# Kernel tuning notes

Measured on AMD Instinct MI355X. Metric: run time of the kernel, lower is better.

Reference implementation:

```python
import jax, jax.numpy as jnp
import numpy as np

EMBED_DIM = 128
N_HEADS = 8
TANH_CLIP = 10.0
NEG_INF = -1e9


def setup_inputs() -> dict:
    key = jax.random.key(0)
    k1, k2, k3, k4 = jax.random.split(key, 4)
    B, N, D = 512, 200, EMBED_DIM
    s = 1.0 / np.sqrt(D)
    return {
        "embeddings": jax.random.normal(k1, (B, N, D), dtype=jnp.float32),
        "W_node": jax.random.uniform(k2, (D, 3 * D), jnp.float32, -s, s),
        "W_fixed": jax.random.uniform(k3, (D, D), jnp.float32, -s, s),
        "W_step": jax.random.uniform(k4, (D, D), jnp.float32, -s, s),
    }


def _decode(embeddings, W_node, W_fixed, W_step):
    B, N, D = embeddings.shape
    H = N_HEADS
    dk = D // H

    # Precompute (once): glimpse K/V and logit K, plus fixed graph context.
    proj = embeddings @ W_node                      # [B,N,3D]
    gK, gV, lK = jnp.split(proj, 3, axis=-1)
    gK = gK.reshape(B, N, H, dk).transpose(0, 2, 1, 3)   # [B,H,N,dk]
    gV = gV.reshape(B, N, H, dk).transpose(0, 2, 1, 3)   # [B,H,N,dk]
    graph_emb = embeddings.mean(axis=1)             # [B,D]
    fixed_ctx = graph_emb @ W_fixed                 # [B,D]

    inv_sqrt_dk = 1.0 / jnp.sqrt(jnp.asarray(dk, embeddings.dtype))
    inv_sqrt_d = 1.0 / jnp.sqrt(jnp.asarray(D, embeddings.dtype))
    batch_idx = jnp.arange(B)

    def step(carry, _):
        visited, ctx_emb = carry                    # [B,N] bool, [B,D]
        q = fixed_ctx + ctx_emb @ W_step            # [B,D]
        qh = q.reshape(B, H, dk)                    # [B,H,dk]
        # glimpse multi-head attention (mask_inner=True)
        compat = jnp.einsum('bhd,bhnd->bhn', qh, gK) * inv_sqrt_dk
        compat = jnp.where(visited[:, None, :], NEG_INF, compat)
        attn = jax.nn.softmax(compat, axis=-1)
        glimpse = jnp.einsum('bhn,bhnd->bhd', attn, gV).reshape(B, D)
        # single-head logits with tanh clipping (mask_logits=True)
        logits = jnp.einsum('bd,bnd->bn', glimpse, lK) * inv_sqrt_d
        logits = TANH_CLIP * jnp.tanh(logits)
        logits = jnp.where(visited, NEG_INF, logits)
        log_p = jax.nn.log_softmax(logits, axis=-1)  # [B,N]
        sel = jnp.argmax(log_p, axis=-1)             # greedy [B]
        visited = visited.at[batch_idx, sel].set(True)
        ctx_emb = embeddings[batch_idx, sel]         # next step context
        return (visited, ctx_emb), (log_p, sel)

    init = (jnp.zeros((B, N), dtype=bool), graph_emb)
    _, (log_ps, sels) = jax.lax.scan(step, init, None, length=N)
    return log_ps.transpose(1, 0, 2), sels.transpose(1, 0)  # [B,T,N], [B,T]


def reference(embeddings, W_node, W_fixed, W_step):
    log_p, pi = _decode(embeddings, W_node, W_fixed, W_step)
    return log_p, pi
```

## Files before the change

### kernel.cpp

```cpp
#include <hip/hip_runtime.h>
#include <math.h>


#define Bsz 512
#define Nn  200
#define Dd  128
#define TANH_CLIP 10.0f
#define NEG_INF  -1e9f
#define LOG2E 1.4426950408889634f
#define LN2   0.6931471805599453f
#define QSCALE (0.25f * LOG2E)
#define LSCALE (0.08838834764831845f * 2.0f * LOG2E)

typedef float v2f __attribute__((ext_vector_type(2)));

__device__ __forceinline__ v2f pkfma(v2f a, v2f b, v2f c) {
    return __builtin_elementwise_fma(a, b, c);
}
__device__ __forceinline__ float fast_rcp(float x) { return __builtin_amdgcn_rcpf(x); }
__device__ __forceinline__ float rdlane(float v, int l) {
    union { float f; int i; } u; u.f = v;
    u.i = __builtin_amdgcn_readlane(u.i, l);
    return u.f;
}

template <int CTRL, int RMASK, bool BC>
__device__ __forceinline__ float dppf(float x, float oldv) {
    int r = __builtin_amdgcn_update_dpp(__builtin_bit_cast(int, oldv),
                                        __builtin_bit_cast(int, x),
                                        CTRL, RMASK, 0xf, BC);
    return __builtin_bit_cast(float, r);
}
template <int CTRL, int RMASK, bool BC>
__device__ __forceinline__ int dppi(int x, int oldv) {
    return __builtin_amdgcn_update_dpp(oldv, x, CTRL, RMASK, 0xf, BC);
}
__device__ __forceinline__ float wave_sum63(float x) {
    x += dppf<0x111, 0xf, true >(x, 0.f);
    x += dppf<0x112, 0xf, true >(x, 0.f);
    x += dppf<0x114, 0xf, true >(x, 0.f);
    x += dppf<0x118, 0xf, true >(x, 0.f);
    x += dppf<0x142, 0xa, false>(x, 0.f);
    x += dppf<0x143, 0xc, false>(x, 0.f);
    return x;
}
__device__ __forceinline__ float wave_max63(float x) {
    x = fmaxf(x, dppf<0x111, 0xf, false>(x, -INFINITY));
    x = fmaxf(x, dppf<0x112, 0xf, false>(x, -INFINITY));
    x = fmaxf(x, dppf<0x114, 0xf, false>(x, -INFINITY));
    x = fmaxf(x, dppf<0x118, 0xf, false>(x, -INFINITY));
    x = fmaxf(x, dppf<0x142, 0xa, false>(x, -INFINITY));
    x = fmaxf(x, dppf<0x143, 0xc, false>(x, -INFINITY));
    return x;
}

__device__ __forceinline__ float dot16pk(const float4* g4, const float4* q4) {
    const v2f* g = (const v2f*)g4;
    const v2f* q = (const v2f*)q4;
    v2f a0 = g[0] * q[0];
    v2f a1 = g[1] * q[1];
    a0 = pkfma(g[2], q[2], a0);
    a1 = pkfma(g[3], q[3], a1);
    a0 = pkfma(g[4], q[4], a0);
    a1 = pkfma(g[5], q[5], a1);
    a0 = pkfma(g[6], q[6], a0);
    a1 = pkfma(g[7], q[7], a1);
    const v2f a = a0 + a1;
    return a.x + a.y;
}

__global__ __launch_bounds__(256, 3) void proj_kernel(
    const float* __restrict__ emb, const float* __restrict__ Wn,
    float* __restrict__ gk, float* __restrict__ gv, float* __restrict__ lk)
{
    const int bid = blockIdx.x;
    const int cg  = bid % 3;
    const int rowBase = (bid / 3) * 64;
    const int t  = threadIdx.x;
    const int c4 = t & 31;
    const int r8 = t >> 5;

    __shared__ __align__(16) float wn_s[64][128];
    __shared__ __align__(16) float e_s[64][68];

    float acc[8][4];
#pragma unroll
    for (int j = 0; j < 8; ++j)
#pragma unroll
        for (int m = 0; m < 4; ++m) acc[j][m] = 0.f;

    for (int kh = 0; kh < 2; ++kh) {
#pragma unroll
        for (int i = 0; i < 8; ++i) {
            const int idx = t + 256 * i;
            const int kr = idx >> 5, cc = (idx & 31) * 4;
            *(float4*)&wn_s[kr][cc] =
                *(const float4*)&Wn[(size_t)(kh * 64 + kr) * 384 + 128 * cg + cc];
        }
#pragma unroll
        for (int i = 0; i < 4; ++i) {
            const int idx = t + 256 * i;
            const int rr = idx >> 4, kk4 = (idx & 15) * 4;
            *(float4*)&e_s[rr][kk4] =
                *(const float4*)&emb[(size_t)(rowBase + rr) * Dd + kh * 64 + kk4];
        }
        __syncthreads();

#pragma unroll
        for (int k4 = 0; k4 < 16; ++k4) {
            float4 er[8];
#pragma unroll
            for (int j = 0; j < 8; ++j)
                er[j] = *(const float4*)&e_s[8 * r8 + j][4 * k4];
#pragma unroll
            for (int m = 0; m < 4; ++m) {
                const float4 wv = *(const float4*)&wn_s[4 * k4 + m][4 * c4];
#pragma unroll
                for (int j = 0; j < 8; ++j) {
                    const float ev = (m == 0) ? er[j].x : (m == 1) ? er[j].y
                                   : (m == 2) ? er[j].z : er[j].w;
                    acc[j][0] = fmaf(ev, wv.x, acc[j][0]);
                    acc[j][1] = fmaf(ev, wv.y, acc[j][1]);
                    acc[j][2] = fmaf(ev, wv.z, acc[j][2]);
                    acc[j][3] = fmaf(ev, wv.w, acc[j][3]);
                }
            }
        }
        __syncthreads();
    }

    float* out = (cg == 0) ? gk : (cg == 1) ? gv : lk;
    const float scl = (cg == 0) ? QSCALE : (cg == 2) ? LSCALE : 1.0f;
#pragma unroll
    for (int j = 0; j < 8; ++j) {
        float4 v;
        v.x = acc[j][0] * scl; v.y = acc[j][1] * scl;
        v.z = acc[j][2] * scl; v.w = acc[j][3] * scl;
        *(float4*)&out[(size_t)(rowBase + 8 * r8 + j) * Dd + 4 * c4] = v;
    }
}

__global__ __launch_bounds__(512, 2) void decode_kernel(
    const float* __restrict__ emb,
    const float* __restrict__ Wf,
    const float* __restrict__ Wsp,
    const float* __restrict__ gk, const float* __restrict__ gv,
    const float* __restrict__ lk,
    float* __restrict__ out_logp,
    float* __restrict__ out_pi)
{
    const int b    = blockIdx.x;
    const int t    = threadIdx.x;
    const int lane = t & 63;
    const int w    = t >> 6;
    const int g    = t >> 7;
    const int d    = t & 127;

    __shared__ __align__(16) float qall_s[201 * Dd];
    __shared__ __align__(16) float wchunk_s[16][Dd];
    __shared__ __align__(16) float red[4][Dd];
    __shared__ __align__(16) float ctx0_s[Dd];
    __shared__ __align__(16) float fixedc_s[Dd];
    __shared__             float smp[256 * 9];
    __shared__ __align__(16) float4 cand[8];

    const float* embB = emb + (size_t)b * Nn * Dd;
    const float* gkB  = gk  + (size_t)b * Nn * Dd;
    const float* gvB  = gv  + (size_t)b * Nn * Dd;
    const float* lkB  = lk  + (size_t)b * Nn * Dd;

    {
        const float4* e4  = (const float4*)embB;
        float4*       es4 = (float4*)qall_s;
#pragma unroll
        for (int it = 0; it < 12; ++it) es4[t + 512 * it] = e4[t + 512 * it];
        if (t < 256) es4[t + 6144] = e4[t + 6144];
    }
    __syncthreads();
    {
        float s = 0.f;
#pragma unroll
        for (int k = 0; k < 50; ++k) s += qall_s[(50 * g + k) * Dd + d];
        red[g][d] = s;
    }
    __syncthreads();
    if (t < 128) ctx0_s[t] = (red[0][t] + red[1][t] + red[2][t] + red[3][t]) * (1.0f / 200.0f);
    __syncthreads();
    {
        float s = 0.f;
#pragma unroll
        for (int j = 0; j < 32; ++j)
            s = fmaf(ctx0_s[32 * g + j], Wf[(32 * g + j) * Dd + d], s);
        red[g][d] = s;
    }
    __syncthreads();
    if (t < 128) {
        fixedc_s[t] = red[0][t] + red[1][t] + red[2][t] + red[3][t];
        qall_s[200 * Dd + t] = ctx0_s[t];
    }
    __syncthreads();

    float qr[52];
#pragma unroll
    for (int i = 0; i < 52; ++i) qr[i] = 0.f;
    for (int kc = 0; kc < 8; ++kc) {
        {
            const int kr = t >> 5, cc = (t & 31) * 4;
            *(float4*)&wchunk_s[kr][cc] =
                *(const float4*)&Wsp[(size_t)(16 * kc + kr) * Dd + cc];
        }
        __syncthreads();
#pragma unroll
        for (int i = 0; i < 52; ++i) {
            const int r = 52 * g + i;
            if (r < 201) {
#pragma unroll
                for (int j4 = 0; j4 < 4; ++j4) {
                    const float4 ev = *(const float4*)&qall_s[r * Dd + 16 * kc + 4 * j4];
                    qr[i] = fmaf(ev.x, wchunk_s[4 * j4 + 0][d], qr[i]);
                    qr[i] = fmaf(ev.y, wchunk_s[4 * j4 + 1][d], qr[i]);
                    qr[i] = fmaf(ev.z, wchunk_s[4 * j4 + 2][d], qr[i]);
                    qr[i] = fmaf(ev.w, wchunk_s[4 * j4 + 3][d], qr[i]);
                }
            }
        }
        __syncthreads();
    }
#pragma unroll
    for (int i = 0; i < 52; ++i) {
        const int r = 52 * g + i;
        if (r < 201) qall_s[r * Dd + d] = qr[i];
    }
    __syncthreads();

    float4 gk0[4], gk1[4], gk2[4], gk3[4];
    float4 lr[4][4];
    float4 vr[4][4];
    float  cb[4];
    {
        const int n3 = (lane < 8) ? lane + 192 : 199;
        const float4* s0 = (const float4*)(gkB + (size_t)(lane      ) * Dd + 16 * w);
        const float4* s1 = (const float4*)(gkB + (size_t)(lane +  64) * Dd + 16 * w);
        const float4* s2 = (const float4*)(gkB + (size_t)(lane + 128) * Dd + 16 * w);
        const float4* s3 = (const float4*)(gkB + (size_t)n3 * Dd + 16 * w);
#pragma unroll
        for (int i = 0; i < 4; ++i) { gk0[i]=s0[i]; gk1[i]=s1[i]; gk2[i]=s2[i]; gk3[i]=s3[i]; }
        const float4* l0 = (const float4*)(lkB + (size_t)(lane      ) * Dd + 16 * w);
        const float4* l1 = (const float4*)(lkB + (size_t)(lane +  64) * Dd + 16 * w);
        const float4* l2 = (const float4*)(lkB + (size_t)(lane + 128) * Dd + 16 * w);
        const float4* l3 = (const float4*)(lkB + (size_t)n3 * Dd + 16 * w);
#pragma unroll
        for (int i = 0; i < 4; ++i) { lr[0][i]=l0[i]; lr[1][i]=l1[i]; lr[2][i]=l2[i]; lr[3][i]=l3[i]; }
        const float4* v0 = (const float4*)(gvB + (size_t)(lane      ) * Dd + 16 * w);
        const float4* v1 = (const float4*)(gvB + (size_t)(lane +  64) * Dd + 16 * w);
        const float4* v2 = (const float4*)(gvB + (size_t)(lane + 128) * Dd + 16 * w);
        const float4* v3 = (const float4*)(gvB + (size_t)n3 * Dd + 16 * w);
#pragma unroll
        for (int i = 0; i < 4; ++i) { vr[0][i]=v0[i]; vr[1][i]=v1[i]; vr[2][i]=v2[i]; vr[3][i]=v3[i]; }
    }
    {
        float4 fcf[4];
        const float4* fcp = (const float4*)(fixedc_s + 16 * w);
#pragma unroll
        for (int i = 0; i < 4; ++i) fcf[i] = fcp[i];
        cb[0] = dot16pk(gk0, fcf);
        cb[1] = dot16pk(gk1, fcf);
        cb[2] = dot16pk(gk2, fcf);
        cb[3] = dot16pk(gk3, fcf);
    }

    const int nB = 32 * w + (lane >> 1);
    const int hB = lane & 1;

    unsigned int visA = 0;
    unsigned int visB = 0;
    int sel_prev = 200;

    for (int step = 0; step < Nn; ++step) {
        float4 qv[4];
        {
            const float4* qp = (const float4*)(qall_s + sel_prev * Dd + 16 * w);
            qv[0] = qp[0]; qv[1] = qp[1]; qv[2] = qp[2]; qv[3] = qp[3];
        }
        float pk4[4];
        {
            float x0 = dot16pk(gk0, qv) + cb[0];
            float x1 = dot16pk(gk1, qv) + cb[1];
            float x2 = dot16pk(gk2, qv) + cb[2];
            float x3 = dot16pk(gk3, qv) + cb[3];
            x0 = (visA & 1u) ? -1e30f : x0;
            x1 = (visA & 2u) ? -1e30f : x1;
            x2 = (visA & 4u) ? -1e30f : x2;
            x3 = (lane < 8 && !(visA & 8u)) ? x3 : -1e30f;
            pk4[0] = exp2f(x0); pk4[1] = exp2f(x1);
            pk4[2] = exp2f(x2); pk4[3] = exp2f(x3);
        }
        v2f gacc[8];
#pragma unroll
        for (int i = 0; i < 8; ++i) gacc[i] = (v2f){0.f, 0.f};
#pragma unroll
        for (int k = 0; k < 4; ++k) {
            const v2f pp = (v2f){pk4[k], pk4[k]};
#pragma unroll
            for (int i = 0; i < 4; ++i) {
                const float4 v = vr[k][i];
                gacc[2*i+0] = pkfma((v2f){v.x, v.y}, pp, gacc[2*i+0]);
                gacc[2*i+1] = pkfma((v2f){v.z, v.w}, pp, gacc[2*i+1]);
            }
        }
        float sgl[16];
        float invps;
        {
            float pssum = wave_sum63((pk4[0] + pk4[1]) + (pk4[2] + pk4[3]));
#pragma unroll
            for (int i = 0; i < 8; ++i) {
                float ra = wave_sum63(gacc[i].x);
                float rb = wave_sum63(gacc[i].y);
                sgl[2*i]   = rdlane(ra, 63);
                sgl[2*i+1] = rdlane(rb, 63);
            }
            invps = fast_rcp(rdlane(pssum, 63));
        }
        {
            float* sp = smp;
#pragma unroll
            for (int k = 0; k < 4; ++k) {
                float a = 0.f;
#pragma unroll
                for (int i = 0; i < 4; ++i) {
                    const float4 L = lr[k][i];
                    a = fmaf(L.x, sgl[4*i+0], a);
                    a = fmaf(L.y, sgl[4*i+1], a);
                    a = fmaf(L.z, sgl[4*i+2], a);
                    a = fmaf(L.w, sgl[4*i+3], a);
                }
                a *= invps;
                if (k < 3)          sp[(lane + 64*k) * 9 + w] = a;
                else if (lane < 8)  sp[(lane + 192)  * 9 + w] = a;
            }
        }
        __syncthreads();

        float lfin;
        {
            const int base = nB * 9 + 4 * hB;
            float s4 = (smp[base] + smp[base+1]) + (smp[base+2] + smp[base+3]);
            s4 += dppf<0xB1, 0xf, true>(s4, 0.f);
            const float u  = exp2f(s4);
            const float lv = TANH_CLIP - 2.0f * TANH_CLIP * fast_rcp(u + 1.0f);
            lfin = (nB >= Nn) ? -INFINITY : ((visB & 1u) ? NEG_INF : lv);
        }
        const float mx_s = rdlane(wave_max63(lfin), 63);
        const unsigned long long bal = __ballot(lfin == mx_s);
        const int sel_w = 32 * w + (__builtin_ctzll(bal) >> 1);
        float e = (hB == 0) ? exp2f((lfin - 10.f) * LOG2E) : 0.f;
        const float esum_w = wave_sum63(e);
        if (lane == 63) {
            float4 c;
            c.x = mx_s; c.y = __int_as_float(sel_w); c.z = esum_w; c.w = 0.f;
            cand[w] = c;
        }
        __syncthreads();

        int sel; float lse;
        {
            const float4 c = cand[lane & 7];
            float cv = c.x; int ci = __float_as_int(c.y); float ce = c.z;
#define CSTEP(CTRL) { \
            float ov = dppf<CTRL, 0xf, true>(cv, 0.f); \
            int   oi = dppi<CTRL, 0xf, true>(ci, 0);   \
            float oe = dppf<CTRL, 0xf, true>(ce, 0.f); \
            ce += oe; \
            if (ov > cv || (ov == cv && oi < ci)) { cv = ov; ci = oi; } }
            CSTEP(0xB1)
            CSTEP(0x4E)
            CSTEP(0x141)
#undef CSTEP
            sel = ci;
            lse = log2f(ce) * LN2 + 10.f;
        }

        if (hB == 0 && nB < Nn)
            out_logp[((size_t)b * Nn + step) * Nn + nB] = lfin - lse;
        if (t == 0) out_pi[(size_t)b * Nn + step] = (float)sel;

        visA |= (sel == lane)        ? 1u : 0u;
        visA |= (sel == lane + 64)   ? 2u : 0u;
        visA |= (sel == lane + 128)  ? 4u : 0u;
        visA |= (sel == lane + 192)  ? 8u : 0u;
        visB |= (sel == nB)          ? 1u : 0u;
        sel_prev = sel;
    }
}

extern "C" void kernel_launch(void* const* d_in, const int* in_sizes, int n_in,
                              void* d_out, int out_size, void* d_ws, size_t ws_size,
                              hipStream_t stream) {
    (void)in_sizes; (void)n_in; (void)out_size; (void)ws_size;
    const float* emb = (const float*)d_in[0];
    const float* Wn  = (const float*)d_in[1];
    const float* Wf  = (const float*)d_in[2];
    const float* Wsp = (const float*)d_in[3];

    const size_t BND = (size_t)Bsz * Nn * Dd;
    float* gk = (float*)d_ws;
    float* gv = gk + BND;
    float* lk = gv + BND;

    float* out_logp = (float*)d_out;
    float* out_pi   = out_logp + (size_t)Bsz * Nn * Nn;

    proj_kernel<<<(Bsz * Nn / 64) * 3, 256, 0, stream>>>(emb, Wn, gk, gv, lk);
    decode_kernel<<<Bsz, 512, 0, stream>>>(emb, Wf, Wsp, gk, gv, lk,
                                           out_logp, out_pi);
}
```

Measured before the change: 1.124 ms.

## Restructure glimpse attention-value product via LDS-staged probabilities and column-split V

Each wave now writes its softmax numerators to shared memory. Each lane holds a strided column slice of gV, 52 rows for one head dimension, instead of 4 full node rows. The glimpse is then a per-lane dot product plus a 4-lane shuffle reduction, which replaces 16 full-wave DPP reductions and readlanes per step. The ps normaliser now uses xor shuffles, and exp2f/log2f are swapped for raw hardware intrinsics. This adds LDS traffic and relies on in-wave LDS ordering without barriers, and the raw intrinsics skip denormal and range handling.

```diff
diff --git a/kernel.cpp b/kernel.cpp
--- a/kernel.cpp
+++ b/kernel.cpp
@@ -18,6 +18,8 @@
     return __builtin_elementwise_fma(a, b, c);
 }
 __device__ __forceinline__ float fast_rcp(float x) { return __builtin_amdgcn_rcpf(x); }
+__device__ __forceinline__ float fexp2(float x)    { return __builtin_amdgcn_exp2f(x); }
+__device__ __forceinline__ float flog2(float x)    { return __builtin_amdgcn_logf(x); }
 __device__ __forceinline__ float rdlane(float v, int l) {
     union { float f; int i; } u; u.f = v;
     u.i = __builtin_amdgcn_readlane(u.i, l);
@@ -155,12 +157,16 @@
     const int w    = t >> 6;
     const int g    = t >> 7;
     const int d    = t & 127;
+    const int jq   = lane >> 2;
+    const int kk   = lane & 3;
 
     __shared__ __align__(16) float qall_s[201 * Dd];
     __shared__ __align__(16) float wchunk_s[16][Dd];
     __shared__ __align__(16) float red[4][Dd];
     __shared__ __align__(16) float ctx0_s[Dd];
     __shared__ __align__(16) float fixedc_s[Dd];
+    __shared__ __align__(16) float sm2[8][256];
+    __shared__ __align__(16) float glimbc[8][16];
     __shared__             float smp[256 * 9];
     __shared__ __align__(16) float4 cand[8];
 
@@ -235,7 +241,7 @@
 
     float4 gk0[4], gk1[4], gk2[4], gk3[4];
     float4 lr[4][4];
-    float4 vr[4][4];
+    float  gva[52];
     float  cb[4];
     {
         const int n3 = (lane < 8) ? lane + 192 : 199;
@@ -251,12 +257,11 @@
         const float4* l3 = (const float4*)(lkB + (size_t)n3 * Dd + 16 * w);
 #pragma unroll
         for (int i = 0; i < 4; ++i) { lr[0][i]=l0[i]; lr[1][i]=l1[i]; lr[2][i]=l2[i]; lr[3][i]=l3[i]; }
-        const float4* v0 = (const float4*)(gvB + (size_t)(lane      ) * Dd + 16 * w);
-        const float4* v1 = (const float4*)(gvB + (size_t)(lane +  64) * Dd + 16 * w);
-        const float4* v2 = (const float4*)(gvB + (size_t)(lane + 128) * Dd + 16 * w);
-        const float4* v3 = (const float4*)(gvB + (size_t)n3 * Dd + 16 * w);
-#pragma unroll
-        for (int i = 0; i < 4; ++i) { vr[0][i]=v0[i]; vr[1][i]=v1[i]; vr[2][i]=v2[i]; vr[3][i]=v3[i]; }
+    }
+#pragma unroll
+    for (int k = 0; k < 52; ++k) {
+        int r = 52 * kk + k; r = r < 200 ? r : 199;
+        gva[k] = gvB[(size_t)r * Dd + 16 * w + jq];
     }
     {
         float4 fcf[4];
@@ -282,7 +287,7 @@
             const float4* qp = (const float4*)(qall_s + sel_prev * Dd + 16 * w);
             qv[0] = qp[0]; qv[1] = qp[1]; qv[2] = qp[2]; qv[3] = qp[3];
         }
-        float pk4[4];
+        float p0, p1, p2, p3;
         {
             float x0 = dot16pk(gk0, qv) + cb[0];
             float x1 = dot16pk(gk1, qv) + cb[1];
@@ -292,52 +297,50 @@
             x1 = (visA & 2u) ? -1e30f : x1;
             x2 = (visA & 4u) ? -1e30f : x2;
             x3 = (lane < 8 && !(visA & 8u)) ? x3 : -1e30f;
-            pk4[0] = exp2f(x0); pk4[1] = exp2f(x1);
-            pk4[2] = exp2f(x2); pk4[3] = exp2f(x3);
-        }
-        v2f gacc[8];
-#pragma unroll
-        for (int i = 0; i < 8; ++i) gacc[i] = (v2f){0.f, 0.f};
-#pragma unroll
-        for (int k = 0; k < 4; ++k) {
-            const v2f pp = (v2f){pk4[k], pk4[k]};
-#pragma unroll
-            for (int i = 0; i < 4; ++i) {
-                const float4 v = vr[k][i];
-                gacc[2*i+0] = pkfma((v2f){v.x, v.y}, pp, gacc[2*i+0]);
-                gacc[2*i+1] = pkfma((v2f){v.z, v.w}, pp, gacc[2*i+1]);
+            p0 = fexp2(x0); p1 = fexp2(x1); p2 = fexp2(x2); p3 = fexp2(x3);
+        }
+        {
+            float* prow = &sm2[w][0];
+            prow[lane      ] = p0;
+            prow[lane +  64] = p1;
+            prow[lane + 128] = p2;
+            prow[lane + 192] = p3;
+        }
+        float ps = (p0 + p1) + (p2 + p3);
+#pragma unroll
+        for (int off = 1; off < 64; off <<= 1) ps += __shfl_xor(ps, off);
+        const float invps = fast_rcp(ps);
+
+        {
+            const float4* a4  = (const float4*)(&sm2[w][52 * kk]);
+            float s0 = 0.f, s1 = 0.f, s2 = 0.f, s3 = 0.f;
+#pragma unroll
+            for (int k4 = 0; k4 < 13; ++k4) {
+                const float4 av = a4[k4];
+                s0 = fmaf(av.x, gva[4 * k4 + 0], s0);
+                s1 = fmaf(av.y, gva[4 * k4 + 1], s1);
+                s2 = fmaf(av.z, gva[4 * k4 + 2], s2);
+                s3 = fmaf(av.w, gva[4 * k4 + 3], s3);
             }
-        }
-        float sgl[16];
-        float invps;
-        {
-            float pssum = wave_sum63((pk4[0] + pk4[1]) + (pk4[2] + pk4[3]));
-#pragma unroll
-            for (int i = 0; i < 8; ++i) {
-                float ra = wave_sum63(gacc[i].x);
-                float rb = wave_sum63(gacc[i].y);
-                sgl[2*i]   = rdlane(ra, 63);
-                sgl[2*i+1] = rdlane(rb, 63);
-            }
-            invps = fast_rcp(rdlane(pssum, 63));
-        }
-        {
-            float* sp = smp;
-#pragma unroll
-            for (int k = 0; k < 4; ++k) {
-                float a = 0.f;
-#pragma unroll
-                for (int i = 0; i < 4; ++i) {
-                    const float4 L = lr[k][i];
-                    a = fmaf(L.x, sgl[4*i+0], a);
-                    a = fmaf(L.y, sgl[4*i+1], a);
-                    a = fmaf(L.z, sgl[4*i+2], a);
-                    a = fmaf(L.w, sgl[4*i+3], a);
-                }
-                a *= invps;
-                if (k < 3)          sp[(lane + 64*k) * 9 + w] = a;
-                else if (lane < 8)  sp[(lane + 192)  * 9 + w] = a;
-            }
+            float gsum = (s0 + s1) + (s2 + s3);
+            gsum += __shfl_xor(gsum, 1);
+            gsum += __shfl_xor(gsum, 2);
+            if (kk == 0) glimbc[w][jq] = gsum * invps;
+        }
+        float4 gw[4];
+        {
+            const float4* gbp = (const float4*)&glimbc[w][0];
+            gw[0] = gbp[0]; gw[1] = gbp[1]; gw[2] = gbp[2]; gw[3] = gbp[3];
+        }
+        {
+            const float a0 = dot16pk(lr[0], gw);
+            const float a1 = dot16pk(lr[1], gw);
+            const float a2 = dot16pk(lr[2], gw);
+            const float a3 = dot16pk(lr[3], gw);
+            smp[(lane      ) * 9 + w] = a0;
+            smp[(lane +  64) * 9 + w] = a1;
+            smp[(lane + 128) * 9 + w] = a2;
+            if (lane < 8) smp[(lane + 192) * 9 + w] = a3;
         }
         __syncthreads();
 
@@ -346,14 +349,14 @@
             const int base = nB * 9 + 4 * hB;
             float s4 = (smp[base] + smp[base+1]) + (smp[base+2] + smp[base+3]);
             s4 += dppf<0xB1, 0xf, true>(s4, 0.f);
-            const float u  = exp2f(s4);
+            const float u  = fexp2(s4);
             const float lv = TANH_CLIP - 2.0f * TANH_CLIP * fast_rcp(u + 1.0f);
             lfin = (nB >= Nn) ? -INFINITY : ((visB & 1u) ? NEG_INF : lv);
         }
         const float mx_s = rdlane(wave_max63(lfin), 63);
         const unsigned long long bal = __ballot(lfin == mx_s);
         const int sel_w = 32 * w + (__builtin_ctzll(bal) >> 1);
-        float e = (hB == 0) ? exp2f((lfin - 10.f) * LOG2E) : 0.f;
+        float e = (hB == 0) ? fexp2((lfin - 10.f) * LOG2E) : 0.f;
         const float esum_w = wave_sum63(e);
         if (lane == 63) {
             float4 c;
@@ -377,7 +380,7 @@
             CSTEP(0x141)
 #undef CSTEP
             sel = ci;
-            lse = log2f(ce) * LN2 + 10.f;
+            lse = flog2(ce) * LN2 + 10.f;
         }
 
         if (hB == 0 && nB < Nn)
```

Measured after the change: 952.8 us. -15.2%, faster.
